# Kernel optimization log

Hardware: AMD Instinct MI355X
Metric: run time of the kernel (lower is better)

## Reference

```python
import jax, jax.numpy as jnp
import numpy as np

NUM_EXPERTS = 64
TOP_K = 2
AUX_COEF = 0.001
Z_COEF = 0.001


def setup_inputs() -> dict:
    key = jax.random.key(0)
    k1, k2 = jax.random.split(key)
    hidden_states = jax.random.normal(k1, (16384, 4096), dtype=jnp.float32)
    W_gate = jax.random.normal(k2, (NUM_EXPERTS, 4096), dtype=jnp.float32) * 0.02
    return {"hidden_states": hidden_states, "W_gate": W_gate}


def reference(hidden_states, W_gate):
    # Gate GEMM: [N, H] x [E, H]^T -> [N, E]
    router_logits = jnp.einsum('nh,eh->ne', hidden_states, W_gate)
    router_probs = jax.nn.softmax(router_logits, axis=-1)

    # Top-k selection + renormalization
    expert_weights, expert_indices = jax.lax.top_k(router_probs, TOP_K)
    expert_weights = expert_weights / jnp.sum(expert_weights, axis=-1, keepdims=True)

    # Load-balancing loss: num_experts * sum_i f_i * P_i
    num_tokens = router_probs.shape[0]
    one_hot = jax.nn.one_hot(expert_indices, NUM_EXPERTS, dtype=jnp.float32)  # [N, K, E]
    tokens_per_expert = one_hot.sum(axis=(0, 1))  # [E]
    f = tokens_per_expert / (num_tokens * TOP_K)
    P = router_probs.mean(axis=0)
    lb_loss = NUM_EXPERTS * jnp.sum(f * P)

    # Z-loss: mean of logsumexp(logits)^2
    log_z = jax.nn.logsumexp(router_logits, axis=-1)
    z_loss = jnp.mean(log_z ** 2)

    aux_loss = AUX_COEF * lb_loss + Z_COEF * z_loss
    return expert_weights, expert_indices, aux_loss
```

## Files before the change

### kernel.cpp

```cpp
#include <hip/hip_runtime.h>
#include <hip/hip_bf16.h>

#define NTOK 16384
#define HD   4096
#define NE   64
#define TTILE 32
#define NBLK (NTOK / TTILE)

typedef __bf16 bf16x8 __attribute__((ext_vector_type(8)));
typedef __bf16 bf16x4 __attribute__((ext_vector_type(4)));
typedef float  f32x4  __attribute__((ext_vector_type(4)));

__device__ __forceinline__ f32x4 mfma16(bf16x8 a, bf16x8 b, f32x4 c) {
    return __builtin_amdgcn_mfma_f32_16x16x32_bf16(a, b, c, 0, 0, 0);
}

#define SAB 40
#define SL  68

__device__ __forceinline__ void cvt_split(float4 v, bf16x4& hi, bf16x4& lo) {
    float x[4] = {v.x, v.y, v.z, v.w};
    #pragma unroll
    for (int e = 0; e < 4; ++e) {
        __bf16 h = (__bf16)x[e];
        hi[e] = h;
        lo[e] = (__bf16)(x[e] - (float)h);
    }
}

__global__ void zero_ws_kernel(float* ws) {
    int i = threadIdx.x;
    if (i < 129) ws[i] = 0.0f;
}

__global__ __launch_bounds__(256) void router_kernel(
    const float* __restrict__ hs,
    const float* __restrict__ Wg,
    float* __restrict__ out,
    float* __restrict__ ws)
{
    __shared__ __bf16 sAhi[2][TTILE * SAB];
    __shared__ __bf16 sAlo[2][TTILE * SAB];
    __shared__ __bf16 sBhi[2][NE * SAB];
    __shared__ __bf16 sBlo[2][NE * SAB];
    __shared__ float  sLog[TTILE * SL];
    __shared__ float  sInv[TTILE];
    __shared__ float  sPp[4 * 64];
    __shared__ float  sCnt[64];
    __shared__ float  sZ;

    const int tid = threadIdx.x;
    const int t0  = blockIdx.x * TTILE;

    if (tid < 64) sCnt[tid] = 0.0f;
    if (tid == 0) sZ = 0.0f;

    const int r1 = tid >> 3;
    const int c4 = (tid & 7) * 4;
    const float* gA = hs + (size_t)(t0 + r1) * HD + c4;
    const float* gB = Wg + (size_t)r1 * HD + c4;
    const int oA  = r1 * SAB + c4;
    const int oB1 = r1 * SAB + c4;
    const int oB2 = (r1 + 32) * SAB + c4;

    const int lane = tid & 63;
    const int wv   = tid >> 6;
    const int wr   = (wv >> 1) * 16;
    const int wc   = (wv & 1) * 32;
    const int fm   = lane & 15;
    const int fq   = lane >> 4;
    const int fk   = fq * 8;

    f32x4 acc[2];
    acc[0] = (f32x4){0.f, 0.f, 0.f, 0.f};
    acc[1] = (f32x4){0.f, 0.f, 0.f, 0.f};

    {
        float4 a0 = *(const float4*)(gA);
        float4 b0 = *(const float4*)(gB);
        float4 b1 = *(const float4*)(gB + 32 * HD);
        bf16x4 h, l;
        cvt_split(a0, h, l); *(bf16x4*)&sAhi[0][oA]  = h; *(bf16x4*)&sAlo[0][oA]  = l;
        cvt_split(b0, h, l); *(bf16x4*)&sBhi[0][oB1] = h; *(bf16x4*)&sBlo[0][oB1] = l;
        cvt_split(b1, h, l); *(bf16x4*)&sBhi[0][oB2] = h; *(bf16x4*)&sBlo[0][oB2] = l;
    }
    __syncthreads();

    const int NIT = HD / 32;
    for (int it = 0; it < NIT; ++it) {
        const int cur = it & 1;
        const bool more = (it + 1) < NIT;
        float4 na0, nb0, nb1;
        if (more) {
            const int k0 = (it + 1) * 32;
            na0 = *(const float4*)(gA + k0);
            nb0 = *(const float4*)(gB + k0);
            nb1 = *(const float4*)(gB + 32 * HD + k0);
        }

        bf16x8 ahi, alo, bhi[2], blo[2];
        {
            const int aoff = (wr + fm) * SAB + fk;
            ahi = *(const bf16x8*)&sAhi[cur][aoff];
            alo = *(const bf16x8*)&sAlo[cur][aoff];
        }
        #pragma unroll
        for (int j = 0; j < 2; ++j) {
            const int boff = (wc + j * 16 + fm) * SAB + fk;
            bhi[j] = *(const bf16x8*)&sBhi[cur][boff];
            blo[j] = *(const bf16x8*)&sBlo[cur][boff];
        }
        #pragma unroll
        for (int j = 0; j < 2; ++j) {
            acc[j] = mfma16(ahi, bhi[j], acc[j]);
            acc[j] = mfma16(ahi, blo[j], acc[j]);
            acc[j] = mfma16(alo, bhi[j], acc[j]);
            acc[j] = mfma16(alo, blo[j], acc[j]);
        }

        if (more) {
            const int nb = cur ^ 1;
            bf16x4 h, l;
            cvt_split(na0, h, l); *(bf16x4*)&sAhi[nb][oA]  = h; *(bf16x4*)&sAlo[nb][oA]  = l;
            cvt_split(nb0, h, l); *(bf16x4*)&sBhi[nb][oB1] = h; *(bf16x4*)&sBlo[nb][oB1] = l;
            cvt_split(nb1, h, l); *(bf16x4*)&sBhi[nb][oB2] = h; *(bf16x4*)&sBlo[nb][oB2] = l;
        }
        __syncthreads();
    }

    #pragma unroll
    for (int j = 0; j < 2; ++j)
        #pragma unroll
        for (int r = 0; r < 4; ++r) {
            const int tokl = wr + fq * 4 + r;
            const int expl = wc + j * 16 + fm;
            sLog[tokl * SL + expl] = acc[j][r];
        }
    __syncthreads();

    const int g = tid >> 3;
    const int l = tid & 7;
    float* Lrow = &sLog[g * SL + l * 8];
    float lv[8];
    float m = -3.0e38f;
    #pragma unroll
    for (int c = 0; c < 8; ++c) { lv[c] = Lrow[c]; m = fmaxf(m, lv[c]); }
    m = fmaxf(m, __shfl_xor(m, 1, 64));
    m = fmaxf(m, __shfl_xor(m, 2, 64));
    m = fmaxf(m, __shfl_xor(m, 4, 64));

    float v1 = -3.0e38f, v2 = -3.0e38f; int i1 = 0, i2 = 0;
    float ssum = 0.0f;
    #pragma unroll
    for (int c = 0; c < 8; ++c) {
        const float val = lv[c]; const int idx = l * 8 + c;
        const float ev = __expf(val - m);
        Lrow[c] = ev;
        ssum += ev;
        if (val > v1) { v2 = v1; i2 = i1; v1 = val; i1 = idx; }
        else if (val > v2) { v2 = val; i2 = idx; }
    }
    ssum += __shfl_xor(ssum, 1, 64);
    ssum += __shfl_xor(ssum, 2, 64);
    ssum += __shfl_xor(ssum, 4, 64);

    #pragma unroll
    for (int s = 1; s <= 4; s <<= 1) {
        const float ov1 = __shfl_xor(v1, s, 64);
        const int   oi1 = __shfl_xor(i1, s, 64);
        const float ov2 = __shfl_xor(v2, s, 64);
        const int   oi2 = __shfl_xor(i2, s, 64);
        float n1, n2; int ni1, ni2;
        const bool ofirst = (ov1 > v1) || (ov1 == v1 && oi1 < i1);
        if (ofirst) {
            n1 = ov1; ni1 = oi1;
            const bool osec = (ov2 > v1) || (ov2 == v1 && oi2 < i1);
            n2 = osec ? ov2 : v1; ni2 = osec ? oi2 : i1;
        } else {
            n1 = v1; ni1 = i1;
            const bool asec = (v2 > ov1) || (v2 == ov1 && i2 < oi1);
            n2 = asec ? v2 : ov1; ni2 = asec ? i2 : oi1;
        }
        v1 = n1; i1 = ni1; v2 = n2; i2 = ni2;
    }

    if (l == 0) {
        const float e1 = __expf(v1 - m), e2 = __expf(v2 - m);
        const float winv = 1.0f / (e1 + e2);
        const int token = t0 + g;
        out[2 * token]     = e1 * winv;
        out[2 * token + 1] = e2 * winv;
        out[2 * NTOK + 2 * token]     = (float)i1;
        out[2 * NTOK + 2 * token + 1] = (float)i2;
        const float lse = m + __logf(ssum);
        atomicAdd(&sZ, lse * lse);
        atomicAdd(&sCnt[i1], 1.0f);
        atomicAdd(&sCnt[i2], 1.0f);
        sInv[g] = 1.0f / ssum;
    }
    __syncthreads();

    {
        const int e = tid & 63;
        const int q = tid >> 6;
        float part = 0.0f;
        #pragma unroll
        for (int t = 0; t < 8; ++t) {
            const int tok = q * 8 + t;
            part += sLog[tok * SL + e] * sInv[tok];
        }
        sPp[q * 64 + e] = part;
    }
    __syncthreads();
    if (tid < 64) {
        const float ps = sPp[tid] + sPp[64 + tid] + sPp[128 + tid] + sPp[192 + tid];
        atomicAdd(&ws[tid], ps);
        atomicAdd(&ws[64 + tid], sCnt[tid]);
    }
    if (tid == 0) atomicAdd(&ws[128], sZ);
}

__global__ void finalize_kernel(const float* __restrict__ ws, float* __restrict__ out) {
    const int e = threadIdx.x;
    const float P = ws[e] * (1.0f / NTOK);
    const float f = ws[64 + e] * (1.0f / (NTOK * 2));
    float term = f * P;
    #pragma unroll
    for (int s = 32; s >= 1; s >>= 1) term += __shfl_xor(term, s, 64);
    if (e == 0) {
        const float lb = 64.0f * term;
        const float z  = ws[128] * (1.0f / NTOK);
        out[4 * NTOK] = 0.001f * lb + 0.001f * z;
    }
}

extern "C" void kernel_launch(void* const* d_in, const int* in_sizes, int n_in,
                              void* d_out, int out_size, void* d_ws, size_t ws_size,
                              hipStream_t stream) {
    const float* hs = (const float*)d_in[0];
    const float* Wg = (const float*)d_in[1];
    float* out = (float*)d_out;
    float* ws  = (float*)d_ws;

    hipLaunchKernelGGL(zero_ws_kernel, dim3(1), dim3(256), 0, stream, ws);
    hipLaunchKernelGGL(router_kernel, dim3(NBLK), dim3(256), 0, stream, hs, Wg, out, ws);
    hipLaunchKernelGGL(finalize_kernel, dim3(1), dim3(64), 0, stream, ws, out);
}
```

Baseline: 415.6 us.

## Pre-split gate weights to bf16 hi/lo and split K across waves without LDS staging

A prep kernel now converts W_gate once per call into an interleaved bf16 hi/lo fragment layout in the workspace. The router kernel drops LDS double-buffering and per-iteration barriers. Each block handles 16 tokens, each wave takes a quarter of K, and fragments are loaded straight from global memory into registers, with a shared-memory reduction across waves afterwards. This removes the repeated weight conversion and the sync overhead. The cost is twice as many blocks re-reading the 1 MB of pre-split weights from L2, plus an extra cross-wave reduction pass.

Result: slower. 430.8 us (+3.6%).

```diff
diff --git a/kernel.cpp b/kernel.cpp
--- a/kernel.cpp
+++ b/kernel.cpp
@@ -4,156 +4,145 @@
 #define NTOK 16384
 #define HD   4096
 #define NE   64
-#define TTILE 32
-#define NBLK (NTOK / TTILE)
+#define KSPLIT 4
+#define KS    (HD / KSPLIT)
+#define NSTEP (KS / 32)
+#define SL2   68
+#define W2OFF 256
+#define W2JSTR 131072
 
 typedef __bf16 bf16x8 __attribute__((ext_vector_type(8)));
-typedef __bf16 bf16x4 __attribute__((ext_vector_type(4)));
 typedef float  f32x4  __attribute__((ext_vector_type(4)));
 
 __device__ __forceinline__ f32x4 mfma16(bf16x8 a, bf16x8 b, f32x4 c) {
     return __builtin_amdgcn_mfma_f32_16x16x32_bf16(a, b, c, 0, 0, 0);
 }
 
-#define SAB 40
-#define SL  68
-
-__device__ __forceinline__ void cvt_split(float4 v, bf16x4& hi, bf16x4& lo) {
-    float x[4] = {v.x, v.y, v.z, v.w};
-    #pragma unroll
-    for (int e = 0; e < 4; ++e) {
-        __bf16 h = (__bf16)x[e];
+__global__ void prep_kernel(const float* __restrict__ Wg, float* __restrict__ ws) {
+    const int idx = blockIdx.x * 256 + threadIdx.x;
+    if (blockIdx.x == 0 && threadIdx.x < 129) ws[threadIdx.x] = 0.0f;
+    __bf16* W2 = (__bf16*)(ws + W2OFF);
+    const float4* src = (const float4*)(Wg + (size_t)idx * 8);
+    float4 q0 = src[0], q1 = src[1];
+    float xs[8] = {q0.x, q0.y, q0.z, q0.w, q1.x, q1.y, q1.z, q1.w};
+    bf16x8 hi, lo;
+    #pragma unroll
+    for (int e = 0; e < 8; ++e) {
+        __bf16 h = (__bf16)xs[e];
         hi[e] = h;
-        lo[e] = (__bf16)(x[e] - (float)h);
-    }
-}
-
-__global__ void zero_ws_kernel(float* ws) {
-    int i = threadIdx.x;
-    if (i < 129) ws[i] = 0.0f;
-}
-
-__global__ __launch_bounds__(256) void router_kernel(
+        lo[e] = (__bf16)(xs[e] - (float)h);
+    }
+    *(bf16x8*)(W2 + (size_t)idx * 16)     = hi;
+    *(bf16x8*)(W2 + (size_t)idx * 16 + 8) = lo;
+}
+
+__global__ __launch_bounds__(256, 4) void router_kernel(
     const float* __restrict__ hs,
-    const float* __restrict__ Wg,
     float* __restrict__ out,
     float* __restrict__ ws)
 {
-    __shared__ __bf16 sAhi[2][TTILE * SAB];
-    __shared__ __bf16 sAlo[2][TTILE * SAB];
-    __shared__ __bf16 sBhi[2][NE * SAB];
-    __shared__ __bf16 sBlo[2][NE * SAB];
-    __shared__ float  sLog[TTILE * SL];
-    __shared__ float  sInv[TTILE];
-    __shared__ float  sPp[4 * 64];
-    __shared__ float  sCnt[64];
-    __shared__ float  sZ;
-
-    const int tid = threadIdx.x;
-    const int t0  = blockIdx.x * TTILE;
+    __shared__ float sRed[4 * 16 * SL2];
+    __shared__ float sInv[16];
+    __shared__ float sPp[256];
+    __shared__ float sCnt[64];
+    __shared__ float sZ;
+
+    const int tid  = threadIdx.x;
+    const int t0   = blockIdx.x * 16;
+    const int wv   = tid >> 6;
+    const int lane = tid & 63;
+    const int fm   = lane & 15;
+    const int fq   = lane >> 4;
 
     if (tid < 64) sCnt[tid] = 0.0f;
     if (tid == 0) sZ = 0.0f;
 
-    const int r1 = tid >> 3;
-    const int c4 = (tid & 7) * 4;
-    const float* gA = hs + (size_t)(t0 + r1) * HD + c4;
-    const float* gB = Wg + (size_t)r1 * HD + c4;
-    const int oA  = r1 * SAB + c4;
-    const int oB1 = r1 * SAB + c4;
-    const int oB2 = (r1 + 32) * SAB + c4;
-
-    const int lane = tid & 63;
-    const int wv   = tid >> 6;
-    const int wr   = (wv >> 1) * 16;
-    const int wc   = (wv & 1) * 32;
-    const int fm   = lane & 15;
-    const int fq   = lane >> 4;
-    const int fk   = fq * 8;
-
-    f32x4 acc[2];
-    acc[0] = (f32x4){0.f, 0.f, 0.f, 0.f};
-    acc[1] = (f32x4){0.f, 0.f, 0.f, 0.f};
+    const __bf16* W2 = (const __bf16*)(ws + W2OFF);
+    const int k0 = wv * KS;
+    const float* aPtr = hs + (size_t)(t0 + fm) * HD + k0 + fq * 8;
+    const int bOff = (fm * 512 + (k0 >> 3) + fq) * 16;
+
+    f32x4 acc[4];
+    #pragma unroll
+    for (int j = 0; j < 4; ++j) acc[j] = (f32x4){0.f, 0.f, 0.f, 0.f};
+
+    float4 a_raw[2][2];
+    bf16x8 b_frag[2][4][2];
+
+    a_raw[0][0] = *(const float4*)(aPtr);
+    a_raw[0][1] = *(const float4*)(aPtr + 4);
+    #pragma unroll
+    for (int j = 0; j < 4; ++j) {
+        const __bf16* bp = W2 + j * W2JSTR + bOff;
+        b_frag[0][j][0] = *(const bf16x8*)(bp);
+        b_frag[0][j][1] = *(const bf16x8*)(bp + 8);
+    }
+
+    #pragma unroll 2
+    for (int it = 0; it < NSTEP; ++it) {
+        const int cur = it & 1, nxt = cur ^ 1;
+        if (it + 1 < NSTEP) {
+            const float* ap = aPtr + (it + 1) * 32;
+            a_raw[nxt][0] = *(const float4*)(ap);
+            a_raw[nxt][1] = *(const float4*)(ap + 4);
+            const __bf16* bp = W2 + bOff + (it + 1) * 64;
+            #pragma unroll
+            for (int j = 0; j < 4; ++j) {
+                b_frag[nxt][j][0] = *(const bf16x8*)(bp + j * W2JSTR);
+                b_frag[nxt][j][1] = *(const bf16x8*)(bp + j * W2JSTR + 8);
+            }
+        }
+        float4 q0 = a_raw[cur][0], q1 = a_raw[cur][1];
+        float xs[8] = {q0.x, q0.y, q0.z, q0.w, q1.x, q1.y, q1.z, q1.w};
+        bf16x8 ahi, alo;
+        #pragma unroll
+        for (int e = 0; e < 8; ++e) {
+            __bf16 h = (__bf16)xs[e];
+            ahi[e] = h;
+            alo[e] = (__bf16)(xs[e] - (float)h);
+        }
+        #pragma unroll
+        for (int j = 0; j < 4; ++j) {
+            acc[j] = mfma16(ahi, b_frag[cur][j][0], acc[j]);
+            acc[j] = mfma16(alo, b_frag[cur][j][0], acc[j]);
+            acc[j] = mfma16(ahi, b_frag[cur][j][1], acc[j]);
+            acc[j] = mfma16(alo, b_frag[cur][j][1], acc[j]);
+        }
+    }
 
     {
-        float4 a0 = *(const float4*)(gA);
-        float4 b0 = *(const float4*)(gB);
-        float4 b1 = *(const float4*)(gB + 32 * HD);
-        bf16x4 h, l;
-        cvt_split(a0, h, l); *(bf16x4*)&sAhi[0][oA]  = h; *(bf16x4*)&sAlo[0][oA]  = l;
-        cvt_split(b0, h, l); *(bf16x4*)&sBhi[0][oB1] = h; *(bf16x4*)&sBlo[0][oB1] = l;
-        cvt_split(b1, h, l); *(bf16x4*)&sBhi[0][oB2] = h; *(bf16x4*)&sBlo[0][oB2] = l;
-    }
-    __syncthreads();
-
-    const int NIT = HD / 32;
-    for (int it = 0; it < NIT; ++it) {
-        const int cur = it & 1;
-        const bool more = (it + 1) < NIT;
-        float4 na0, nb0, nb1;
-        if (more) {
-            const int k0 = (it + 1) * 32;
-            na0 = *(const float4*)(gA + k0);
-            nb0 = *(const float4*)(gB + k0);
-            nb1 = *(const float4*)(gB + 32 * HD + k0);
-        }
-
-        bf16x8 ahi, alo, bhi[2], blo[2];
-        {
-            const int aoff = (wr + fm) * SAB + fk;
-            ahi = *(const bf16x8*)&sAhi[cur][aoff];
-            alo = *(const bf16x8*)&sAlo[cur][aoff];
-        }
-        #pragma unroll
-        for (int j = 0; j < 2; ++j) {
-            const int boff = (wc + j * 16 + fm) * SAB + fk;
-            bhi[j] = *(const bf16x8*)&sBhi[cur][boff];
-            blo[j] = *(const bf16x8*)&sBlo[cur][boff];
-        }
-        #pragma unroll
-        for (int j = 0; j < 2; ++j) {
-            acc[j] = mfma16(ahi, bhi[j], acc[j]);
-            acc[j] = mfma16(ahi, blo[j], acc[j]);
-            acc[j] = mfma16(alo, bhi[j], acc[j]);
-            acc[j] = mfma16(alo, blo[j], acc[j]);
-        }
-
-        if (more) {
-            const int nb = cur ^ 1;
-            bf16x4 h, l;
-            cvt_split(na0, h, l); *(bf16x4*)&sAhi[nb][oA]  = h; *(bf16x4*)&sAlo[nb][oA]  = l;
-            cvt_split(nb0, h, l); *(bf16x4*)&sBhi[nb][oB1] = h; *(bf16x4*)&sBlo[nb][oB1] = l;
-            cvt_split(nb1, h, l); *(bf16x4*)&sBhi[nb][oB2] = h; *(bf16x4*)&sBlo[nb][oB2] = l;
-        }
-        __syncthreads();
-    }
-
-    #pragma unroll
-    for (int j = 0; j < 2; ++j)
-        #pragma unroll
-        for (int r = 0; r < 4; ++r) {
-            const int tokl = wr + fq * 4 + r;
-            const int expl = wc + j * 16 + fm;
-            sLog[tokl * SL + expl] = acc[j][r];
-        }
-    __syncthreads();
-
-    const int g = tid >> 3;
-    const int l = tid & 7;
-    float* Lrow = &sLog[g * SL + l * 8];
-    float lv[8];
+        float* my = &sRed[wv * 16 * SL2];
+        #pragma unroll
+        for (int j = 0; j < 4; ++j)
+            #pragma unroll
+            for (int r = 0; r < 4; ++r)
+                my[(fq * 4 + r) * SL2 + (j * 16 + fm)] = acc[j][r];
+    }
+    __syncthreads();
+    for (int s = tid; s < 1024; s += 256) {
+        const int t = s >> 6, e = s & 63;
+        const int o = t * SL2 + e;
+        sRed[o] = sRed[o] + sRed[16 * SL2 + o] + sRed[32 * SL2 + o] + sRed[48 * SL2 + o];
+    }
+    __syncthreads();
+
+    const int g = tid >> 4;
+    const int l = tid & 15;
+    float* Lrow = &sRed[g * SL2 + l * 4];
+    float lv[4];
     float m = -3.0e38f;
     #pragma unroll
-    for (int c = 0; c < 8; ++c) { lv[c] = Lrow[c]; m = fmaxf(m, lv[c]); }
+    for (int c = 0; c < 4; ++c) { lv[c] = Lrow[c]; m = fmaxf(m, lv[c]); }
     m = fmaxf(m, __shfl_xor(m, 1, 64));
     m = fmaxf(m, __shfl_xor(m, 2, 64));
     m = fmaxf(m, __shfl_xor(m, 4, 64));
+    m = fmaxf(m, __shfl_xor(m, 8, 64));
 
     float v1 = -3.0e38f, v2 = -3.0e38f; int i1 = 0, i2 = 0;
     float ssum = 0.0f;
     #pragma unroll
-    for (int c = 0; c < 8; ++c) {
-        const float val = lv[c]; const int idx = l * 8 + c;
+    for (int c = 0; c < 4; ++c) {
+        const float val = lv[c]; const int idx = l * 4 + c;
         const float ev = __expf(val - m);
         Lrow[c] = ev;
         ssum += ev;
@@ -163,9 +152,10 @@
     ssum += __shfl_xor(ssum, 1, 64);
     ssum += __shfl_xor(ssum, 2, 64);
     ssum += __shfl_xor(ssum, 4, 64);
-
-    #pragma unroll
-    for (int s = 1; s <= 4; s <<= 1) {
+    ssum += __shfl_xor(ssum, 8, 64);
+
+    #pragma unroll
+    for (int s = 1; s <= 8; s <<= 1) {
         const float ov1 = __shfl_xor(v1, s, 64);
         const int   oi1 = __shfl_xor(i1, s, 64);
         const float ov2 = __shfl_xor(v2, s, 64);
@@ -205,9 +195,9 @@
         const int q = tid >> 6;
         float part = 0.0f;
         #pragma unroll
-        for (int t = 0; t < 8; ++t) {
-            const int tok = q * 8 + t;
-            part += sLog[tok * SL + e] * sInv[tok];
+        for (int t = 0; t < 4; ++t) {
+            const int tok = q * 4 + t;
+            part += sRed[tok * SL2 + e] * sInv[tok];
         }
         sPp[q * 64 + e] = part;
     }
@@ -242,7 +232,7 @@
     float* out = (float*)d_out;
     float* ws  = (float*)d_ws;
 
-    hipLaunchKernelGGL(zero_ws_kernel, dim3(1), dim3(256), 0, stream, ws);
-    hipLaunchKernelGGL(router_kernel, dim3(NBLK), dim3(256), 0, stream, hs, Wg, out, ws);
+    hipLaunchKernelGGL(prep_kernel, dim3(128), dim3(256), 0, stream, Wg, ws);
+    hipLaunchKernelGGL(router_kernel, dim3(NTOK / 16), dim3(256), 0, stream, hs, out, ws);
     hipLaunchKernelGGL(finalize_kernel, dim3(1), dim3(64), 0, stream, ws, out);
 }
```
